# Performance work log

Hardware: AMD Instinct MI355X
Metric: run time of the kernel (lower is better)

The kernel has to match this reference:

```python
import jax, jax.numpy as jnp
import numpy as np

B, N, F_IN, F_HID, F_EMB, H, L_DIM = 8, 1024, 128, 128, 128, 8, 2


def _xavier(key, shape, fan_in, fan_out):
    lim = np.sqrt(6.0 / (fan_in + fan_out))
    return jax.random.uniform(key, shape, jnp.float32, -lim, lim)


def setup_inputs() -> dict:
    key = jax.random.key(0)
    ks = jax.random.split(key, 16)
    x = jax.random.normal(ks[0], (B, N, F_IN), jnp.float32)
    # sparse 0/1 adjacency with self loops (avoids fully-masked softmax rows)
    adj = (jax.random.uniform(ks[1], (B, N, N)) < 0.05).astype(jnp.float32)
    adj = jnp.maximum(adj, jnp.eye(N, dtype=jnp.float32)[None])
    def gat_params(k, f_in, f_out):
        k1, k2, k3 = jax.random.split(k, 3)
        return (_xavier(k1, (H, f_in, f_out), f_in, f_out),
                _xavier(k2, (H, f_out, 1), f_out, 1),
                _xavier(k3, (H, f_out, 1), f_out, 1),
                jnp.zeros((f_out,), jnp.float32))
    w1, as1, ad1, b1 = gat_params(ks[2], F_IN, F_HID)
    w2, as2, ad2, b2 = gat_params(ks[3], F_HID, F_HID)
    w3, as3, ad3, b3 = gat_params(ks[4], F_HID, F_EMB)
    pred_in = F_HID * 2 + F_EMB  # hidden*(num_layers-1)+embedding, concat=True
    pw = _xavier(ks[5], (pred_in, L_DIM), pred_in, L_DIM)
    pb = jnp.zeros((L_DIM,), jnp.float32)
    return {"x": x, "adj": adj,
            "w1": w1, "as1": as1, "ad1": ad1, "b1": b1,
            "w2": w2, "as2": as2, "ad2": ad2, "b2": b2,
            "w3": w3, "as3": as3, "ad3": ad3, "b3": b3,
            "pw": pw, "pb": pb}


def gat_layer(h, adj, w, a_src, a_dst, bias):
    # h: [B,N,f_in] -> h_prime: [B,H,N,f_out]
    hp = jnp.einsum('bnf,hfo->bhno', h, w)
    t = jnp.tanh(hp)
    s = jnp.einsum('bhno,hoi->bhni', t, a_src)[..., 0]  # [B,H,N]
    d = jnp.einsum('bhno,hoi->bhni', t, a_dst)[..., 0]  # [B,H,N]
    scores = s[:, :, :, None] + d[:, :, None, :]        # [B,H,N,N]
    scores = jnp.where(scores >= 0, scores, 0.2 * scores)  # LeakyReLU(0.2)
    scores = jnp.where(adj[:, None, :, :] > 0, scores, -jnp.inf)
    attn = jax.nn.softmax(scores, axis=-1)  # dropout disabled (eval mode)
    out = jnp.einsum('bhnm,bhmo->bhno', attn, hp) + bias
    return out.mean(axis=1)  # merge heads -> [B,N,f_out]


def reference(x, adj, w1, as1, ad1, b1, w2, as2, ad2, b2, w3, as3, ad3, b3, pw, pb):
    x1 = jax.nn.relu(gat_layer(x, adj, w1, as1, ad1, b1))
    x2 = jax.nn.relu(gat_layer(x1, adj, w2, as2, ad2, b2))
    x3 = gat_layer(x2, adj, w3, as3, ad3, b3)
    x_all = jnp.concatenate([x1, x2, x3], axis=2)  # [B,N,pred_in]
    pooled = jnp.max(x_all, axis=1)                # max over nodes -> [B,pred_in]
    return pooled @ pw + pb                        # [B,label_dim]
```

## Files before the change

kernel.cpp:

```cpp
#include <hip/hip_runtime.h>
#include <hip/hip_fp16.h>

#define BB 8
#define NN 1024
#define FF 128
#define HH 8

typedef _Float16 f16;
typedef f16  f16x8 __attribute__((ext_vector_type(8)));
typedef f16  f16x4 __attribute__((ext_vector_type(4)));
typedef float f32x4 __attribute__((ext_vector_type(4)));

#define L2E 1.44269504f

__global__ void k_pre(const float* __restrict__ x, f16* __restrict__ x16a,
                      const float* __restrict__ w1, const float* __restrict__ w2,
                      const float* __restrict__ w3, f16* __restrict__ wB,
                      const float* __restrict__ adj, unsigned* __restrict__ am){
  int bid = blockIdx.x, t = threadIdx.x;
  if (bid < 512){
    int i = (bid*256 + t)*8;
    float4 a = *(const float4*)(x+i), b = *(const float4*)(x+i+4);
    f16x8 v;
    v[0]=(f16)a.x; v[1]=(f16)a.y; v[2]=(f16)a.z; v[3]=(f16)a.w;
    v[4]=(f16)b.x; v[5]=(f16)b.y; v[6]=(f16)b.z; v[7]=(f16)b.w;
    *(f16x8*)(x16a+i) = v;
  } else if (bid < 704){
    int e = (bid-512)*256 + t;
    int fc = e & 15, c = (e>>4)&127, h = (e>>11)&7, l = e>>14;
    const float* w = (l==0) ? w1 : ((l==1) ? w2 : w3);
    f16x8 v;
    #pragma unroll
    for(int j=0;j<8;j++) v[j] = (f16)w[(h*128 + fc*8 + j)*128 + c];
    *(f16x8*)(wB + (((l*8+h)*16 + fc)*128 + c)*8) = v;
  } else {
    int wv = t >> 6, lane = t & 63;
    int r = (bid-704)*4 + wv;
    const float* row = adj + (long)r*1024;
    for(int g=0; g<16; g++){
      float v = row[g*64 + lane];
      unsigned long long mb = __ballot(v > 0.0f);
      if (lane == 0){
        am[r*32 + 2*g]   = (unsigned)mb;
        am[r*32 + 2*g+1] = (unsigned)(mb >> 32);
      }
    }
  }
}

__global__ __launch_bounds__(256,2) void k_hp(
    const f16* __restrict__ xin,
    const f16* __restrict__ wBl,
    const float* __restrict__ asrc, const float* __restrict__ adst,
    f16* __restrict__ hpB,
    float* __restrict__ sarr, float* __restrict__ darr)
{
  __shared__ f16 xs[128*136];
  __shared__ float asl[128], adl[128];
  int t = threadIdx.x;
  int bid = blockIdx.x;
  int h = bid & 7, it = (bid>>3)&7, b = bid>>6;
  int i0 = it*128;
  {
    const f16* src = xin + (long)(b*1024 + i0)*128;
    int fc = t & 15, r0 = t >> 4;
    #pragma unroll
    for(int p=0;p<8;p++){
      int r = r0 + p*16;
      f16x8 v = *(const f16x8*)(src + r*128 + fc*8);
      *(f16x8*)(xs + r*136 + fc*8) = v;
    }
  }
  if (t < 128){ asl[t] = asrc[h*128+t]; adl[t] = adst[h*128+t]; }
  __syncthreads();

  int lane = t & 63, wv = t>>6, wr = wv>>1, wc = wv&1;
  int mq = lane & 15, quad = lane >> 4;
  f32x4 acc[4][4];
  #pragma unroll
  for(int a=0;a<4;a++)
    #pragma unroll
    for(int c=0;c<4;c++) acc[a][c] = (f32x4){0.f,0.f,0.f,0.f};

  const f16* wh = wBl + h*16*128*8;
  #pragma unroll
  for(int ks=0; ks<4; ks++){
    f16x8 af[4], bf[4];
    #pragma unroll
    for(int mt=0; mt<4; mt++)
      af[mt] = *(const f16x8*)(xs + (wr*64 + mt*16 + mq)*136 + ks*32 + quad*8);
    #pragma unroll
    for(int nt=0; nt<4; nt++){
      int c  = wc*64 + nt*16 + mq;
      int fc = ks*4 + quad;
      bf[nt] = *(const f16x8*)(wh + (fc*128 + c)*8);
    }
    #pragma unroll
    for(int mt=0; mt<4; mt++)
      #pragma unroll
      for(int nt=0; nt<4; nt++)
        acc[mt][nt] = __builtin_amdgcn_mfma_f32_16x16x32_f16(af[mt], bf[nt], acc[mt][nt], 0,0,0);
  }
  __syncthreads();
  f16* tt = xs;
  f16* hpb = hpB + (long)(b*8+h)*128*128*8;
  #pragma unroll
  for(int mt=0; mt<4; mt++){
    #pragma unroll
    for(int nt=0; nt<4; nt++){
      int c = wc*64 + nt*16 + mq;
      f16x4 pk;
      #pragma unroll
      for(int rg=0; rg<4; rg++){
        float v = acc[mt][nt][rg];
        pk[rg] = (f16)v;
        int il = wr*64 + mt*16 + quad*4 + rg;
        float e2 = __expf(2.0f*v);
        float th = 1.0f - 2.0f*__builtin_amdgcn_rcpf(e2 + 1.0f);
        tt[il*136 + c] = (f16)th;
      }
      int il0 = wr*64 + mt*16 + quad*4;
      int inode = i0 + il0;
      *(f16x4*)(hpb + ((long)(inode>>3)*128 + c)*8 + (inode&7)) = pk;
    }
  }
  __syncthreads();
  {
    int r = t>>1, hf = t&1;
    float s_p = 0.f, d_p = 0.f;
    #pragma unroll
    for(int q=0;q<8;q++){
      f16x8 tv = *(const f16x8*)(tt + r*136 + hf*64 + q*8);
      #pragma unroll
      for(int j=0;j<8;j++){
        float tvf = (float)tv[j];
        int c = hf*64 + q*8 + j;
        s_p = fmaf(tvf, asl[c], s_p);
        d_p = fmaf(tvf, adl[c], d_p);
      }
    }
    s_p += __shfl_xor(s_p, 1);
    d_p += __shfl_xor(d_p, 1);
    if (hf == 0){
      sarr[(b*8+h)*1024 + i0 + r] = s_p;
      darr[(b*8+h)*1024 + i0 + r] = d_p;
    }
  }
}

__global__ __launch_bounds__(256,4) void k_attn(
    const f16* __restrict__ hpB,
    const float* __restrict__ sarr, const float* __restrict__ darr,
    const unsigned* __restrict__ am,
    f16* __restrict__ part)
{
  __shared__ float ddl[1024];
  __shared__ float wred[4];
  __shared__ float zl[64];
  __shared__ f16 Pl[2][64*72];
  int t = threadIdx.x;
  int bid = blockIdx.x;
  int bh = bid & 63, it = bid >> 6;
  int i0 = it*64;
  int b = bh >> 3;

  int lane = t&63, wv = t>>6;
  int mq = lane&15, quad = lane>>4;
  const f16* hpb = hpB + (long)bh*128*128*8;

  {
    float4 v = *(const float4*)(darr + bh*1024 + t*4);
    float mx = fmaxf(fmaxf(v.x,v.y), fmaxf(v.z,v.w));
    #pragma unroll
    for(int o=1;o<64;o<<=1) mx = fmaxf(mx, __shfl_xor(mx, o));
    if (lane == 0) wred[wv] = mx;
    *(float4*)(ddl + t*4) = make_float4(v.x*L2E, v.y*L2E, v.z*L2E, v.w*L2E);
  }

  int prow = t>>2, pg = t&3;
  float srowl = sarr[bh*1024 + i0 + prow] * L2E;
  const unsigned* amrow = am + ((long)(b*1024 + i0 + prow))*32;
  int wsel = pg >> 1, wsh = (pg&1)*16;

  f16x8 bcur[4], bnx[4];
  #pragma unroll
  for(int kk=0;kk<2;kk++)
    #pragma unroll
    for(int nt=0;nt<2;nt++){
      int c  = wv*32 + nt*16 + mq;
      int jc = kk*4 + quad;
      bcur[kk*2+nt] = *(const f16x8*)(hpb + ((long)jc*128 + c)*8);
    }
  unsigned wcur = amrow[wsel];
  unsigned wnx  = amrow[2 + wsel];

  __syncthreads();
  float Dml = fmaxf(fmaxf(wred[0],wred[1]), fmaxf(wred[2],wred[3])) * L2E;
  float ml = srowl + Dml;
  float mrowl = fmaxf(ml, 0.2f*ml);

  f32x4 acc[4][2];
  #pragma unroll
  for(int a=0;a<4;a++){ acc[a][0] = (f32x4){0.f,0.f,0.f,0.f}; acc[a][1] = (f32x4){0.f,0.f,0.f,0.f}; }
  float zacc = 0.f;
  f16x8 zerov = (f16x8){0,0,0,0,0,0,0,0};

#define PFILL(BUF, WORDSRC, DBASE)                                        \
  {                                                                       \
    f16* myp = Pl[BUF] + prow*72 + pg*16;                                 \
    *(f16x8*)myp = zerov; *(f16x8*)(myp+8) = zerov;                       \
    unsigned word = ((WORDSRC) >> wsh) & 0xffffu;                         \
    const float* dloc = ddl + (DBASE) + pg*16;                            \
    if (word){                                                            \
      int n = __popc(word);                                               \
      unsigned w = word;                                                  \
      int j0 = __builtin_ctz(w); w &= w-1u;                               \
      int j1 = w ? __builtin_ctz(w) : j0; w = w ? (w & (w-1u)) : 0u;      \
      int j2 = w ? __builtin_ctz(w) : j0; w = w ? (w & (w-1u)) : 0u;      \
      int j3 = w ? __builtin_ctz(w) : j0;                                 \
      unsigned wrest = w ? (w & (w-1u)) : 0u;                             \
      float v0 = dloc[j0], v1 = dloc[j1], v2 = dloc[j2], v3 = dloc[j3];   \
      float x0 = srowl+v0, x1 = srowl+v1, x2 = srowl+v2, x3 = srowl+v3;   \
      float e0 = __builtin_amdgcn_exp2f(fmaxf(x0,0.2f*x0) - mrowl);       \
      float e1 = __builtin_amdgcn_exp2f(fmaxf(x1,0.2f*x1) - mrowl);      \
      float e2 = __builtin_amdgcn_exp2f(fmaxf(x2,0.2f*x2) - mrowl);      \
      float e3 = __builtin_amdgcn_exp2f(fmaxf(x3,0.2f*x3) - mrowl);      \
      zacc += e0; myp[j0] = (f16)e0;                                      \
      if (n > 1){ zacc += e1; myp[j1] = (f16)e1; }                        \
      if (n > 2){ zacc += e2; myp[j2] = (f16)e2; }                        \
      if (n > 3){ zacc += e3; myp[j3] = (f16)e3; }                        \
      while (wrest){                                                      \
        int j = __builtin_ctz(wrest); wrest &= wrest-1u;                  \
        float xl = srowl + dloc[j];                                       \
        float e  = __builtin_amdgcn_exp2f(fmaxf(xl,0.2f*xl) - mrowl);     \
        zacc += e; myp[j] = (f16)e;                                       \
      }                                                                   \
    }                                                                     \
  }

  PFILL(0, wcur, 0)
  __syncthreads();

  for(int jt=0; jt<16; jt++){
    if (jt < 15){
      #pragma unroll
      for(int kk=0;kk<2;kk++)
        #pragma unroll
        for(int nt=0;nt<2;nt++){
          int c  = wv*32 + nt*16 + mq;
          int jc = (jt+1)*8 + kk*4 + quad;
          bnx[kk*2+nt] = *(const f16x8*)(hpb + ((long)jc*128 + c)*8);
        }
      unsigned wfut = (jt < 14) ? amrow[(jt+2)*2 + wsel] : 0u;
      PFILL((jt+1)&1, wnx, (jt+1)*64)
      wnx = wfut;
    }
    const f16* Pc = Pl[jt&1];
    #pragma unroll
    for(int kk=0;kk<2;kk++){
      #pragma unroll
      for(int mt=0;mt<4;mt++){
        f16x8 a = *(const f16x8*)(Pc + (mt*16+mq)*72 + kk*32 + quad*8);
        #pragma unroll
        for(int nt=0;nt<2;nt++)
          acc[mt][nt] = __builtin_amdgcn_mfma_f32_16x16x32_f16(a, bcur[kk*2+nt], acc[mt][nt], 0,0,0);
      }
    }
    __syncthreads();
    if (jt < 15){
      #pragma unroll
      for(int q=0;q<4;q++) bcur[q] = bnx[q];
    }
  }
#undef PFILL

  zacc += __shfl_xor(zacc, 1);
  zacc += __shfl_xor(zacc, 2);
  if (pg == 0) zl[prow] = zacc;
  __syncthreads();

  f16* Ps = (f16*)Pl;
  #pragma unroll
  for(int mt=0;mt<4;mt++){
    #pragma unroll
    for(int rg=0;rg<4;rg++){
      int il = mt*16 + quad*4 + rg;
      float zi = 0.125f * __builtin_amdgcn_rcpf(zl[il]);
      #pragma unroll
      for(int nt=0;nt<2;nt++){
        int c = wv*32 + nt*16 + mq;
        Ps[il*136 + c] = (f16)(acc[mt][nt][rg] * zi);
      }
    }
  }
  __syncthreads();
  {
    int r = t>>2, g = t&3;
    f16* dst = part + ((long)bh*1024 + i0 + r)*128 + g*32;
    const f16* srcp = Ps + r*136 + g*32;
    *(f16x8*)(dst)    = *(const f16x8*)(srcp);
    *(f16x8*)(dst+8)  = *(const f16x8*)(srcp+8);
    *(f16x8*)(dst+16) = *(const f16x8*)(srcp+16);
    *(f16x8*)(dst+24) = *(const f16x8*)(srcp+24);
  }
}

__global__ void k_fin(const f16* __restrict__ part, const float* __restrict__ bias,
                      f16* __restrict__ x16, float* __restrict__ pmax, int do_relu){
  __shared__ float pm[16][128];
  int t = threadIdx.x;
  int idx = blockIdx.x*256 + t;
  int c8 = idx & 15, n = (idx>>4)&1023, b = idx>>14;
  float s[8];
  #pragma unroll
  for(int j=0;j<8;j++) s[j] = 0.f;
  #pragma unroll
  for(int h=0;h<8;h++){
    int bh = b*8 + h;
    f16x8 p0 = *(const f16x8*)(part + ((long)bh*1024 + n)*128 + c8*8);
    #pragma unroll
    for(int j=0;j<8;j++) s[j] += (float)p0[j];
  }
  f16x8 h8;
  float ov[8];
  #pragma unroll
  for(int j=0;j<8;j++){
    float v = s[j] + bias[c8*8 + j];
    if (do_relu) v = fmaxf(v, 0.f);
    ov[j] = v;
    h8[j] = (f16)v;
  }
  if (x16) *(f16x8*)(x16 + ((long)(b*1024+n))*128 + c8*8) = h8;
  #pragma unroll
  for(int j=0;j<8;j++) pm[n&15][c8*8+j] = ov[j];
  __syncthreads();
  if (t < 128){
    float m = pm[0][t];
    #pragma unroll
    for(int r=1;r<16;r++) m = fmaxf(m, pm[r][t]);
    pmax[blockIdx.x*128 + t] = m;
  }
}

__global__ void k_pool2(const float* __restrict__ pmax, const float* __restrict__ pw,
                        const float* __restrict__ pb, float* __restrict__ out){
  __shared__ float ph[2][384];
  __shared__ float pl[384];
  int b = blockIdx.x, t = threadIdx.x;
  int c = t & 127, half = t >> 7;
  #pragma unroll
  for(int l=0;l<3;l++){
    const float* p = pmax + l*65536 + b*8192 + half*32*128 + c;
    float m = -3.4e38f;
    #pragma unroll 8
    for(int kk=0;kk<32;kk++) m = fmaxf(m, p[kk*128]);
    ph[half][l*128 + c] = m;
  }
  __syncthreads();
  for(int f = t; f < 384; f += 256) pl[f] = fmaxf(ph[0][f], ph[1][f]);
  __syncthreads();
  if (t < 64){
    float a0 = 0.f, a1 = 0.f;
    #pragma unroll
    for(int k=0;k<6;k++){
      int f = t + 64*k;
      float v = pl[f];
      a0 = fmaf(v, pw[f*2],   a0);
      a1 = fmaf(v, pw[f*2+1], a1);
    }
    #pragma unroll
    for(int o=1;o<64;o<<=1){ a0 += __shfl_xor(a0,o); a1 += __shfl_xor(a1,o); }
    if (t == 0){ out[b*2] = a0 + pb[0]; out[b*2+1] = a1 + pb[1]; }
  }
}

extern "C" void kernel_launch(void* const* d_in, const int* in_sizes, int n_in,
                              void* d_out, int out_size, void* d_ws, size_t ws_size,
                              hipStream_t stream) {
  const float* x   = (const float*)d_in[0];
  const float* adj = (const float*)d_in[1];
  const float* w1  = (const float*)d_in[2];
  const float* as1 = (const float*)d_in[3];
  const float* ad1 = (const float*)d_in[4];
  const float* b1  = (const float*)d_in[5];
  const float* w2  = (const float*)d_in[6];
  const float* as2 = (const float*)d_in[7];
  const float* ad2 = (const float*)d_in[8];
  const float* b2  = (const float*)d_in[9];
  const float* w3  = (const float*)d_in[10];
  const float* as3 = (const float*)d_in[11];
  const float* ad3 = (const float*)d_in[12];
  const float* b3  = (const float*)d_in[13];
  const float* pw  = (const float*)d_in[14];
  const float* pb  = (const float*)d_in[15];

  char* ws = (char*)d_ws;
  f16*      x16a = (f16*)ws;                 ws += (size_t)1048576*2;
  f16*      x16b = (f16*)ws;                 ws += (size_t)1048576*2;
  f16*      wB   = (f16*)ws;                 ws += (size_t)393216*2;
  unsigned* am   = (unsigned*)ws;            ws += (size_t)8*1024*32*4;
  f16*      hpB  = (f16*)ws;                 ws += (size_t)8*8*1024*128*2;
  float*    sarr = (float*)ws;               ws += (size_t)65536*4;
  float*    darr = (float*)ws;               ws += (size_t)65536*4;
  f16*      part = (f16*)ws;                 ws += (size_t)64*1024*128*2;
  float*    pmax = (float*)ws;               ws += (size_t)3*512*128*4;

  k_pre<<<2752, 256, 0, stream>>>(x, x16a, w1, w2, w3, wB, adj, am);

  k_hp  <<<512, 256, 0, stream>>>(x16a, wB,            as1, ad1, hpB, sarr, darr);
  k_attn<<<1024,256, 0, stream>>>(hpB, sarr, darr, am, part);
  k_fin <<<512, 256, 0, stream>>>(part, b1, x16b, pmax,           1);
  k_hp  <<<512, 256, 0, stream>>>(x16b, wB + 131072,   as2, ad2, hpB, sarr, darr);
  k_attn<<<1024,256, 0, stream>>>(hpB, sarr, darr, am, part);
  k_fin <<<512, 256, 0, stream>>>(part, b2, x16a, pmax + 65536,   1);
  k_hp  <<<512, 256, 0, stream>>>(x16a, wB + 262144,   as3, ad3, hpB, sarr, darr);
  k_attn<<<1024,256, 0, stream>>>(hpB, sarr, darr, am, part);
  k_fin <<<512, 256, 0, stream>>>(part, b3, nullptr, pmax + 131072, 0);

  k_pool2<<<8, 256, 0, stream>>>(pmax, pw, pb, (float*)d_out);
}
```

Baseline: 254.9 us.

## Build attention probability fragments in registers instead of shared-memory staging

The sparse softmax probabilities are now computed by each wave directly into its MFMA A-operand registers, packing f16 values into u32x4 fragments by bit-OR. This removes the double-buffered shared-memory P tile and the per-tile __syncthreads. Each wave now redundantly computes exp for all 64 rows (4x the work of the previous cooperative fill), and uses more registers and adds select-heavy insertion logic. Row sums are reduced with cross-lane shuffles instead of through shared memory.

```diff
diff --git a/kernel.cpp b/kernel.cpp
--- a/kernel.cpp
+++ b/kernel.cpp
@@ -10,6 +10,7 @@
 typedef f16  f16x8 __attribute__((ext_vector_type(8)));
 typedef f16  f16x4 __attribute__((ext_vector_type(4)));
 typedef float f32x4 __attribute__((ext_vector_type(4)));
+typedef unsigned u32x4 __attribute__((ext_vector_type(4)));
 
 #define L2E 1.44269504f
 
@@ -156,8 +157,7 @@
 {
   __shared__ float ddl[1024];
   __shared__ float wred[4];
-  __shared__ float zl[64];
-  __shared__ f16 Pl[2][64*72];
+  __shared__ f16 Ps[64*136];
   int t = threadIdx.x;
   int bid = blockIdx.x;
   int bh = bid & 63, it = bid >> 6;
@@ -177,71 +177,106 @@
     *(float4*)(ddl + t*4) = make_float4(v.x*L2E, v.y*L2E, v.z*L2E, v.w*L2E);
   }
 
-  int prow = t>>2, pg = t&3;
-  float srowl = sarr[bh*1024 + i0 + prow] * L2E;
-  const unsigned* amrow = am + ((long)(b*1024 + i0 + prow))*32;
-  int wsel = pg >> 1, wsh = (pg&1)*16;
-
-  f16x8 bcur[4], bnx[4];
+  const unsigned* amq = am + ((long)(b*1024 + i0 + mq))*32;
+
+  uint2 mA[4], mB[4];
+  #pragma unroll
+  for(int mt=0;mt<4;mt++){
+    const unsigned* ar = amq + mt*512;
+    mA[mt] = *(const uint2*)(ar);
+    mB[mt] = *(const uint2*)(ar + 2);
+  }
+  f16x8 bf[4];
   #pragma unroll
   for(int kk=0;kk<2;kk++)
     #pragma unroll
     for(int nt=0;nt<2;nt++){
       int c  = wv*32 + nt*16 + mq;
       int jc = kk*4 + quad;
-      bcur[kk*2+nt] = *(const f16x8*)(hpb + ((long)jc*128 + c)*8);
-    }
-  unsigned wcur = amrow[wsel];
-  unsigned wnx  = amrow[2 + wsel];
+      bf[kk*2+nt] = *(const f16x8*)(hpb + ((long)jc*128 + c)*8);
+    }
 
   __syncthreads();
   float Dml = fmaxf(fmaxf(wred[0],wred[1]), fmaxf(wred[2],wred[3])) * L2E;
-  float ml = srowl + Dml;
-  float mrowl = fmaxf(ml, 0.2f*ml);
+  float srl[4], mrl[4];
+  #pragma unroll
+  for(int mt=0;mt<4;mt++){
+    float s = sarr[bh*1024 + i0 + mt*16 + mq] * L2E;
+    srl[mt] = s;
+    float ml = s + Dml;
+    mrl[mt] = fmaxf(ml, 0.2f*ml);
+  }
 
   f32x4 acc[4][2];
   #pragma unroll
   for(int a=0;a<4;a++){ acc[a][0] = (f32x4){0.f,0.f,0.f,0.f}; acc[a][1] = (f32x4){0.f,0.f,0.f,0.f}; }
-  float zacc = 0.f;
-  f16x8 zerov = (f16x8){0,0,0,0,0,0,0,0};
-
-#define PFILL(BUF, WORDSRC, DBASE)                                        \
-  {                                                                       \
-    f16* myp = Pl[BUF] + prow*72 + pg*16;                                 \
-    *(f16x8*)myp = zerov; *(f16x8*)(myp+8) = zerov;                       \
-    unsigned word = ((WORDSRC) >> wsh) & 0xffffu;                         \
-    const float* dloc = ddl + (DBASE) + pg*16;                            \
-    if (word){                                                            \
-      int n = __popc(word);                                               \
-      unsigned w = word;                                                  \
-      int j0 = __builtin_ctz(w); w &= w-1u;                               \
-      int j1 = w ? __builtin_ctz(w) : j0; w = w ? (w & (w-1u)) : 0u;      \
-      int j2 = w ? __builtin_ctz(w) : j0; w = w ? (w & (w-1u)) : 0u;      \
-      int j3 = w ? __builtin_ctz(w) : j0;                                 \
-      unsigned wrest = w ? (w & (w-1u)) : 0u;                             \
-      float v0 = dloc[j0], v1 = dloc[j1], v2 = dloc[j2], v3 = dloc[j3];   \
-      float x0 = srowl+v0, x1 = srowl+v1, x2 = srowl+v2, x3 = srowl+v3;   \
-      float e0 = __builtin_amdgcn_exp2f(fmaxf(x0,0.2f*x0) - mrowl);       \
-      float e1 = __builtin_amdgcn_exp2f(fmaxf(x1,0.2f*x1) - mrowl);      \
-      float e2 = __builtin_amdgcn_exp2f(fmaxf(x2,0.2f*x2) - mrowl);      \
-      float e3 = __builtin_amdgcn_exp2f(fmaxf(x3,0.2f*x3) - mrowl);      \
-      zacc += e0; myp[j0] = (f16)e0;                                      \
-      if (n > 1){ zacc += e1; myp[j1] = (f16)e1; }                        \
-      if (n > 2){ zacc += e2; myp[j2] = (f16)e2; }                        \
-      if (n > 3){ zacc += e3; myp[j3] = (f16)e3; }                        \
-      while (wrest){                                                      \
-        int j = __builtin_ctz(wrest); wrest &= wrest-1u;                  \
-        float xl = srowl + dloc[j];                                       \
-        float e  = __builtin_amdgcn_exp2f(fmaxf(xl,0.2f*xl) - mrowl);     \
-        zacc += e; myp[j] = (f16)e;                                       \
-      }                                                                   \
-    }                                                                     \
-  }
-
-  PFILL(0, wcur, 0)
-  __syncthreads();
+  float zac[4] = {0.f,0.f,0.f,0.f};
+  const u32x4 zero4 = (u32x4){0u,0u,0u,0u};
+  int sh8 = quad*8;
+
+#define INS(MT, J, E) {                                                        \
+    unsigned hu = (unsigned)__builtin_bit_cast(unsigned short,(f16)(E))        \
+                  << (((J)&1)*16);                                             \
+    int dw = (J)>>1;                                                           \
+    a0[MT][0] |= (dw==0)?hu:0u; a0[MT][1] |= (dw==1)?hu:0u;                    \
+    a0[MT][2] |= (dw==2)?hu:0u; a0[MT][3] |= (dw==3)?hu:0u;                    \
+    a1[MT][0] |= (dw==4)?hu:0u; a1[MT][1] |= (dw==5)?hu:0u;                    \
+    a1[MT][2] |= (dw==6)?hu:0u; a1[MT][3] |= (dw==7)?hu:0u; }
 
   for(int jt=0; jt<16; jt++){
+    u32x4 a0[4], a1[4];
+    #pragma unroll
+    for(int mt=0;mt<4;mt++){ a0[mt]=zero4; a1[mt]=zero4; }
+    const float* dl = ddl + jt*64 + sh8;
+    #pragma unroll
+    for(int mt=0;mt<4;mt++){
+      unsigned w16 = ((mA[mt].x >> sh8) & 0xffu) | (((mA[mt].y >> sh8) & 0xffu) << 8);
+      if (w16){
+        int n = __popc(w16);
+        unsigned w = w16;
+        int j0 = __builtin_ctz(w); w &= w-1u;
+        int j1 = w ? __builtin_ctz(w) : j0; w = w ? (w & (w-1u)) : 0u;
+        int j2 = w ? __builtin_ctz(w) : j0; w = w ? (w & (w-1u)) : 0u;
+        int j3 = w ? __builtin_ctz(w) : j0;
+        unsigned wrest = w ? (w & (w-1u)) : 0u;
+        int o0 = (j0&7) + ((j0>>3)<<5), o1 = (j1&7) + ((j1>>3)<<5);
+        int o2 = (j2&7) + ((j2>>3)<<5), o3 = (j3&7) + ((j3>>3)<<5);
+        float d0 = dl[o0], d1 = dl[o1], d2 = dl[o2], d3 = dl[o3];
+        float x0 = srl[mt]+d0, x1 = srl[mt]+d1, x2 = srl[mt]+d2, x3 = srl[mt]+d3;
+        float e0 = __builtin_amdgcn_exp2f(fmaxf(x0,0.2f*x0) - mrl[mt]);
+        float e1 = __builtin_amdgcn_exp2f(fmaxf(x1,0.2f*x1) - mrl[mt]);
+        float e2 = __builtin_amdgcn_exp2f(fmaxf(x2,0.2f*x2) - mrl[mt]);
+        float e3 = __builtin_amdgcn_exp2f(fmaxf(x3,0.2f*x3) - mrl[mt]);
+        zac[mt] += e0; INS(mt, j0, e0)
+        if (n > 1){ zac[mt] += e1; INS(mt, j1, e1) }
+        if (n > 2){ zac[mt] += e2; INS(mt, j2, e2) }
+        if (n > 3){ zac[mt] += e3; INS(mt, j3, e3) }
+        while (wrest){
+          int j = __builtin_ctz(wrest); wrest &= wrest-1u;
+          int o = (j&7) + ((j>>3)<<5);
+          float xl = srl[mt] + dl[o];
+          float e  = __builtin_amdgcn_exp2f(fmaxf(xl,0.2f*xl) - mrl[mt]);
+          zac[mt] += e; INS(mt, j, e)
+        }
+      }
+    }
+    #pragma unroll
+    for(int kk=0;kk<2;kk++){
+      #pragma unroll
+      for(int mt=0;mt<4;mt++){
+        f16x8 a = __builtin_bit_cast(f16x8, kk ? a1[mt] : a0[mt]);
+        #pragma unroll
+        for(int nt=0;nt<2;nt++)
+          acc[mt][nt] = __builtin_amdgcn_mfma_f32_16x16x32_f16(a, bf[kk*2+nt], acc[mt][nt], 0,0,0);
+      }
+    }
+    #pragma unroll
+    for(int mt=0;mt<4;mt++) mA[mt] = mB[mt];
+    if (jt < 14){
+      #pragma unroll
+      for(int mt=0;mt<4;mt++)
+        mB[mt] = *(const uint2*)(amq + mt*512 + (jt+2)*2);
+    }
     if (jt < 15){
       #pragma unroll
       for(int kk=0;kk<2;kk++)
@@ -249,43 +284,25 @@
         for(int nt=0;nt<2;nt++){
           int c  = wv*32 + nt*16 + mq;
           int jc = (jt+1)*8 + kk*4 + quad;
-          bnx[kk*2+nt] = *(const f16x8*)(hpb + ((long)jc*128 + c)*8);
+          bf[kk*2+nt] = *(const f16x8*)(hpb + ((long)jc*128 + c)*8);
         }
-      unsigned wfut = (jt < 14) ? amrow[(jt+2)*2 + wsel] : 0u;
-      PFILL((jt+1)&1, wnx, (jt+1)*64)
-      wnx = wfut;
-    }
-    const f16* Pc = Pl[jt&1];
-    #pragma unroll
-    for(int kk=0;kk<2;kk++){
-      #pragma unroll
-      for(int mt=0;mt<4;mt++){
-        f16x8 a = *(const f16x8*)(Pc + (mt*16+mq)*72 + kk*32 + quad*8);
-        #pragma unroll
-        for(int nt=0;nt<2;nt++)
-          acc[mt][nt] = __builtin_amdgcn_mfma_f32_16x16x32_f16(a, bcur[kk*2+nt], acc[mt][nt], 0,0,0);
-      }
-    }
-    __syncthreads();
-    if (jt < 15){
-      #pragma unroll
-      for(int q=0;q<4;q++) bcur[q] = bnx[q];
-    }
-  }
-#undef PFILL
-
-  zacc += __shfl_xor(zacc, 1);
-  zacc += __shfl_xor(zacc, 2);
-  if (pg == 0) zl[prow] = zacc;
-  __syncthreads();
-
-  f16* Ps = (f16*)Pl;
+    }
+  }
+#undef INS
+
   #pragma unroll
   for(int mt=0;mt<4;mt++){
+    zac[mt] += __shfl_xor(zac[mt], 16);
+    zac[mt] += __shfl_xor(zac[mt], 32);
+  }
+
+  #pragma unroll
+  for(int mt=0;mt<4;mt++){
     #pragma unroll
     for(int rg=0;rg<4;rg++){
+      float zr = __shfl(zac[mt], quad*4 + rg);
+      float zi = 0.125f * __builtin_amdgcn_rcpf(zr);
       int il = mt*16 + quad*4 + rg;
-      float zi = 0.125f * __builtin_amdgcn_rcpf(zl[il]);
       #pragma unroll
       for(int nt=0;nt<2;nt++){
         int c = wv*32 + nt*16 + mq;
```

After: 421.3 us. +65.3%, slower.
